# Optimization experiments

Hardware: AMD Instinct MI355X
Metric: run time of the kernel (lower is better)

Reference implementation:

```python
import jax, jax.numpy as jnp
import numpy as np

N, D, E_LOCAL, E_GLOBAL = 50000, 128, 500000, 600000


def gcn_conv(x, W, b, src, dst, w, n):
    """PyG GCNConv with add_self_loops=True, symmetric normalization.

    deg[i] = sum of incoming edge weights at i + 1 (self-loop weight 1)
    norm_e = deg^-1/2[src] * w_e * deg^-1/2[dst]
    out[i] = sum_e norm_e * (xW)[src_e]  +  deg^-1[i] * (xW)[i]  + b
    """
    xw = x @ W  # [n, out]
    deg = jax.ops.segment_sum(w, dst, num_segments=n) + 1.0
    dinv = jnp.where(deg > 0, jax.lax.rsqrt(deg), 0.0)
    norm = dinv[src] * w * dinv[dst]  # [E]
    agg = jax.ops.segment_sum(norm[:, None] * xw[src], dst, num_segments=n)
    self_loop = (dinv * dinv)[:, None] * xw
    return agg + self_loop + b


def setup_inputs() -> dict:
    key = jax.random.key(0)
    ks = jax.random.split(key, 10)
    activity = jax.random.normal(ks[0], (N, D), dtype=jnp.float32)
    learning = jax.random.normal(ks[1], (N, D), dtype=jnp.float32)
    edge_index = jax.random.randint(ks[2], (2, E_LOCAL), 0, N, dtype=jnp.int32)
    edge_weight = jax.random.uniform(ks[3], (E_LOCAL,), dtype=jnp.float32)
    global_edge_index = jax.random.randint(ks[4], (2, E_GLOBAL), 0, N, dtype=jnp.int32)
    global_edge_weight = jax.random.uniform(ks[5], (E_GLOBAL,), dtype=jnp.float32)
    s = 1.0 / np.sqrt(D)
    W_local = jax.random.uniform(ks[6], (D, D), jnp.float32, -s, s)
    b_local = jnp.zeros((D,), jnp.float32)
    W_global = jax.random.uniform(ks[7], (D, D), jnp.float32, -s, s)
    b_global = jnp.zeros((D,), jnp.float32)
    return {
        "activity": activity, "learning": learning,
        "edge_index": edge_index, "edge_weight": edge_weight,
        "global_edge_index": global_edge_index, "global_edge_weight": global_edge_weight,
        "W_local": W_local, "b_local": b_local,
        "W_global": W_global, "b_global": b_global,
    }


def reference(activity, learning, edge_index, edge_weight,
              global_edge_index, global_edge_weight,
              W_local, b_local, W_global, b_global):
    n = activity.shape[0]
    xa = activity + learning
    # Note: GCNConv1 branches in the original are dead code (outputs overwritten);
    # only GCNConv2 (local and global) affect the output.
    xl = gcn_conv(xa, W_local, b_local, edge_index[0], edge_index[1], edge_weight, n)
    xg = gcn_conv(xa, W_global, b_global, global_edge_index[0], global_edge_index[1], global_edge_weight, n)
    wei = jax.nn.sigmoid(xl + xg)
    return 2.0 * activity * wei + 2.0 * learning * (1.0 - wei)
```

## Files before the change

### kernel.cpp

```cpp
#include <hip/hip_runtime.h>

#define DFEAT 128
#define EPB 4096
#define MAXBINS 512

typedef __attribute__((ext_vector_type(8))) short short8;
typedef __attribute__((ext_vector_type(4))) float float4v;

__device__ __forceinline__ float bf2f(unsigned int h) {
    union { unsigned int u; float f; } v; v.u = h << 16; return v.f;
}
__device__ __forceinline__ unsigned short f2bf(float f) {
    union { float f; unsigned int u; } v; v.f = f;
    unsigned int u = v.u;
    unsigned int lsb = (u >> 16) & 1u;
    u += 0x7fffu + lsb;
    return (unsigned short)(u >> 16);
}
__device__ __forceinline__ float blo(unsigned int u) {
    union { unsigned int x; float f; } v; v.x = u << 16; return v.f;
}
__device__ __forceinline__ float bhi(unsigned int u) {
    union { unsigned int x; float f; } v; v.x = u & 0xffff0000u; return v.f;
}

__global__ __launch_bounds__(256) void zprep_kernel(
    const float* __restrict__ Wl, const float* __restrict__ Wg,
    unsigned short* __restrict__ WT,
    unsigned int* __restrict__ counts, int nz)
{
    if (blockIdx.x < 128) {
        int idx = blockIdx.x * 256 + threadIdx.x;
        int m = idx >> 14, rem = idx & 16383;
        int k = rem >> 7, c = rem & 127;
        const float* W = m ? Wg : Wl;
        WT[m * 16384 + c * 128 + k] = f2bf(W[k * 128 + c]);
        return;
    }
    int i = (blockIdx.x - 128) * 256 + threadIdx.x;
    if (i < nz) counts[i] = 0u;
}

__global__ __launch_bounds__(256) void gemm_bin1_kernel(
    const float* __restrict__ A, const float* __restrict__ L,
    const unsigned short* __restrict__ WT,
    unsigned short* __restrict__ xwl, unsigned short* __restrict__ xwg,
    const int* __restrict__ dstL, const int* __restrict__ dstG,
    unsigned int* __restrict__ counts,
    int El, int Eg, int n, int GB, int NPB)
{
    __shared__ unsigned int lcnt[MAXBINS];
    if (blockIdx.x >= GB) {
        const int NBINS = (2 * n + 255) >> 8;
        for (int b = threadIdx.x; b < NBINS; b += 256) lcnt[b] = 0u;
        __syncthreads();
        const int k = blockIdx.x - GB;
        const int e0 = k * EPB;
        const int E = El + Eg;
        #pragma unroll
        for (int r = 0; r < EPB / 256; ++r) {
            int e = e0 + r * 256 + threadIdx.x;
            if (e < E) {
                int t = (e < El) ? dstL[e] : n + dstG[e - El];
                atomicAdd(&lcnt[t >> 8], 1u);
            }
        }
        __syncthreads();
        for (int b = threadIdx.x; b < NBINS; b += 256)
            counts[(size_t)b * NPB + k] = lcnt[b];
        return;
    }
    const int tid  = threadIdx.x;
    const int wid  = tid >> 6;
    const int lane = tid & 63;
    const int quad = lane >> 4;
    const int cl   = lane & 15;

    int rowa = blockIdx.x * 64 + wid * 16 + cl;
    if (rowa > n - 1) rowa = n - 1;

    const float* Ar = A + (size_t)rowa * DFEAT;
    const float* Lr = L + (size_t)rowa * DFEAT;

    short8 a[4];
    #pragma unroll
    for (int kk = 0; kk < 4; ++kk) {
        const int kb = kk * 32 + quad * 8;
        float4 a0 = *(const float4*)&Ar[kb];
        float4 a1 = *(const float4*)&Ar[kb + 4];
        float4 l0 = *(const float4*)&Lr[kb];
        float4 l1 = *(const float4*)&Lr[kb + 4];
        union { short8 v; unsigned short u[8]; } s;
        s.u[0] = f2bf(a0.x + l0.x); s.u[1] = f2bf(a0.y + l0.y);
        s.u[2] = f2bf(a0.z + l0.z); s.u[3] = f2bf(a0.w + l0.w);
        s.u[4] = f2bf(a1.x + l1.x); s.u[5] = f2bf(a1.y + l1.y);
        s.u[6] = f2bf(a1.z + l1.z); s.u[7] = f2bf(a1.w + l1.w);
        a[kk] = s.v;
    }

    const int rbase = blockIdx.x * 64 + wid * 16 + quad * 4;
    const char* wtb = (const char*)WT + quad * 16;

    #pragma unroll
    for (int m = 0; m < 2; ++m) {
        unsigned short* out = m ? xwg : xwl;
        #pragma unroll
        for (int t = 0; t < 8; ++t) {
            const int col = t * 16 + cl;
            const char* bp = wtb + m * 32768 + col * 256;
            float4v acc = {0.f, 0.f, 0.f, 0.f};
            #pragma unroll
            for (int kk = 0; kk < 4; ++kk) {
                short8 b = *(const short8*)(bp + kk * 64);
                acc = __builtin_amdgcn_mfma_f32_16x16x32_bf16(a[kk], b, acc, 0, 0, 0);
            }
            #pragma unroll
            for (int r = 0; r < 4; ++r) {
                int ro = rbase + r;
                if (ro < n) out[(size_t)ro * DFEAT + col] = f2bf(acc[r]);
            }
        }
    }
}

__global__ __launch_bounds__(512) void scanA_kernel(unsigned int* __restrict__ counts,
                                                    unsigned int* __restrict__ bintot,
                                                    int NPB)
{
    __shared__ unsigned int tmp[512];
    const int b = blockIdx.x;
    const int i = threadIdx.x;
    unsigned int v = (i < NPB) ? counts[(size_t)b * NPB + i] : 0u;
    tmp[i] = v;
    __syncthreads();
    for (int off = 1; off < 512; off <<= 1) {
        unsigned int t = (i >= off) ? tmp[i - off] : 0u;
        __syncthreads();
        tmp[i] += t;
        __syncthreads();
    }
    if (i < NPB) counts[(size_t)b * NPB + i] = tmp[i] - v;
    if (i == 511) bintot[b] = tmp[511];
}

__global__ __launch_bounds__(512) void scanB_kernel(const unsigned int* __restrict__ bintot,
                                                    unsigned int* __restrict__ binbase,
                                                    int NBINS)
{
    __shared__ unsigned int tmp[512];
    const int i = threadIdx.x;
    unsigned int v = (i < NBINS) ? bintot[i] : 0u;
    tmp[i] = v;
    __syncthreads();
    for (int off = 1; off < 512; off <<= 1) {
        unsigned int t = (i >= off) ? tmp[i - off] : 0u;
        __syncthreads();
        tmp[i] += t;
        __syncthreads();
    }
    if (i < NBINS) binbase[i] = tmp[i] - v;
    if (i == 511) binbase[NBINS] = tmp[511];
}

__global__ __launch_bounds__(256) void scatter_kernel(
    const int* __restrict__ srcL, const int* __restrict__ dstL, const float* __restrict__ wL,
    const int* __restrict__ srcG, const int* __restrict__ dstG, const float* __restrict__ wG,
    const unsigned int* __restrict__ counts, const unsigned int* __restrict__ binbase,
    unsigned int* __restrict__ payload, unsigned char* __restrict__ tloc,
    int El, int Eg, int n, int NPB)
{
    __shared__ unsigned int lbase[MAXBINS];
    __shared__ unsigned int lcnt[MAXBINS];
    const int NBINS = (2 * n + 255) >> 8;
    const int k = blockIdx.x;
    for (int b = threadIdx.x; b < NBINS; b += 256) {
        lbase[b] = binbase[b] + counts[(size_t)b * NPB + k];
        lcnt[b]  = 0u;
    }
    __syncthreads();
    const int e0 = k * EPB;
    const int E = El + Eg;
    #pragma unroll
    for (int r = 0; r < EPB / 256; ++r) {
        int e = e0 + r * 256 + threadIdx.x;
        if (e < E) {
            int s, t; float w;
            if (e < El) { s = srcL[e]; t = dstL[e]; w = wL[e]; }
            else { int e2 = e - El; s = srcG[e2]; t = n + dstG[e2]; w = wG[e2]; }
            const int bin = t >> 8;
            unsigned int rank = atomicAdd(&lcnt[bin], 1u);
            unsigned int pos = lbase[bin] + rank;
            unsigned int wq = (unsigned int)(w * 65535.0f + 0.5f);
            if (wq > 65535u) wq = 65535u;
            payload[pos] = (wq << 16) | (unsigned int)s;
            tloc[pos] = (unsigned char)(t & 255);
        }
    }
}

__global__ __launch_bounds__(256) void binsort_kernel(
    const unsigned int* __restrict__ binbase,
    const unsigned int* __restrict__ payload, const unsigned char* __restrict__ tloc,
    unsigned int* __restrict__ edata, unsigned int* __restrict__ ptrpk,
    float* __restrict__ dinv, int n2)
{
    __shared__ unsigned int cnt[256], wsum[256], off[256], cnt2[256], tmp[256];
    const int b = blockIdx.x;
    const unsigned int s0 = binbase[b], s1 = binbase[b + 1];
    cnt[threadIdx.x] = 0u; wsum[threadIdx.x] = 0u; cnt2[threadIdx.x] = 0u;
    __syncthreads();
    for (unsigned int i = s0 + threadIdx.x; i < s1; i += 256) {
        unsigned int tl = tloc[i];
        atomicAdd(&cnt[tl], 1u);
        atomicAdd(&wsum[tl], payload[i] >> 16);
    }
    __syncthreads();
    unsigned int v = cnt[threadIdx.x];
    tmp[threadIdx.x] = v;
    __syncthreads();
    for (int o = 1; o < 256; o <<= 1) {
        unsigned int t = (threadIdx.x >= o) ? tmp[threadIdx.x - o] : 0u;
        __syncthreads();
        tmp[threadIdx.x] += t;
        __syncthreads();
    }
    off[threadIdx.x] = tmp[threadIdx.x] - v;
    const int t = b * 256 + threadIdx.x;
    if (t < n2) {
        dinv[t]  = rsqrtf((float)wsum[threadIdx.x] * (1.0f / 65535.0f) + 1.0f);
        ptrpk[t] = (s0 + off[threadIdx.x]) | (v << 24);
    }
    __syncthreads();
    for (unsigned int i = s0 + threadIdx.x; i < s1; i += 256) {
        unsigned int tl = tloc[i];
        unsigned int r = atomicAdd(&cnt2[tl], 1u);
        edata[s0 + off[tl] + r] = payload[i];
    }
}

__global__ __launch_bounds__(256) void gather_kernel(
    const unsigned short* __restrict__ xwl, const unsigned short* __restrict__ xwg,
    const unsigned int* __restrict__ ptrpk, const unsigned int* __restrict__ edata,
    const float* __restrict__ dinv,
    const float* __restrict__ A, const float* __restrict__ Lr,
    const float* __restrict__ bl, const float* __restrict__ bg,
    float* __restrict__ out, int n)
{
    const int lane = threadIdx.x & 63;
    const int grp  = lane >> 4;
    const int fl   = lane & 15;
    const int node = blockIdx.x * 4 + (threadIdx.x >> 6);
    if (node >= n) return;

    const unsigned int pl = ptrpk[node];
    const unsigned int pg = ptrpk[n + node];
    const int i0l = (int)(pl & 0xFFFFFFu);
    const int i1l = i0l + (int)(pl >> 24);
    const int i0g = (int)(pg & 0xFFFFFFu);
    const int i1g = i0g + (int)(pg >> 24);
    const float dvl = dinv[node];
    const float dvg = dinv[n + node];
    const float dl = dvl * dvl;
    const float dg = dvg * dvg;
    const float dtl = dvl * (1.0f / 65535.0f);
    const float dtg = dvg * (1.0f / 65535.0f);

    const int fo = fl * 8;
    const size_t nbase = (size_t)node * DFEAT + fo;
    const uint4 svl = *(const uint4*)&xwl[nbase];
    const uint4 svg = *(const uint4*)&xwg[nbase];

    float acc[8] = {0.f, 0.f, 0.f, 0.f, 0.f, 0.f, 0.f, 0.f};

    for (int b0 = i0l; b0 < i1l; b0 += 64) {
        int idx = b0 + lane;
        unsigned int ed = edata[idx < i1l ? idx : (i1l - 1)];
        int   sv  = (int)(ed & 0xFFFFu);
        float nmv = dinv[sv] * (float)(ed >> 16) * dtl;
        int cnt = i1l - b0; if (cnt > 64) cnt = 64;
        int iters = (cnt + 3) >> 2;
        #pragma unroll 4
        for (int jj = 0; jj < iters; ++jj) {
            int sl = 4 * jj + grp;
            float nm = __shfl(nmv, sl);
            int   s  = __shfl(sv,  sl);
            if (sl >= cnt) nm = 0.f;
            uint4 pk = *(const uint4*)&xwl[(size_t)s * DFEAT + fo];
            acc[0] += nm * blo(pk.x); acc[1] += nm * bhi(pk.x);
            acc[2] += nm * blo(pk.y); acc[3] += nm * bhi(pk.y);
            acc[4] += nm * blo(pk.z); acc[5] += nm * bhi(pk.z);
            acc[6] += nm * blo(pk.w); acc[7] += nm * bhi(pk.w);
        }
    }
    for (int b0 = i0g; b0 < i1g; b0 += 64) {
        int idx = b0 + lane;
        unsigned int ed = edata[idx < i1g ? idx : (i1g - 1)];
        int   sv  = (int)(ed & 0xFFFFu);
        float nmv = dinv[n + sv] * (float)(ed >> 16) * dtg;
        int cnt = i1g - b0; if (cnt > 64) cnt = 64;
        int iters = (cnt + 3) >> 2;
        #pragma unroll 4
        for (int jj = 0; jj < iters; ++jj) {
            int sl = 4 * jj + grp;
            float nm = __shfl(nmv, sl);
            int   s  = __shfl(sv,  sl);
            if (sl >= cnt) nm = 0.f;
            uint4 pk = *(const uint4*)&xwg[(size_t)s * DFEAT + fo];
            acc[0] += nm * blo(pk.x); acc[1] += nm * bhi(pk.x);
            acc[2] += nm * blo(pk.y); acc[3] += nm * bhi(pk.y);
            acc[4] += nm * blo(pk.z); acc[5] += nm * bhi(pk.z);
            acc[6] += nm * blo(pk.w); acc[7] += nm * bhi(pk.w);
        }
    }

    #pragma unroll
    for (int j = 0; j < 8; ++j) {
        acc[j] += __shfl_xor(acc[j], 16);
        acc[j] += __shfl_xor(acc[j], 32);
    }

    acc[0] += dl * blo(svl.x) + dg * blo(svg.x);
    acc[1] += dl * bhi(svl.x) + dg * bhi(svg.x);
    acc[2] += dl * blo(svl.y) + dg * blo(svg.y);
    acc[3] += dl * bhi(svl.y) + dg * bhi(svg.y);
    acc[4] += dl * blo(svl.z) + dg * blo(svg.z);
    acc[5] += dl * bhi(svl.z) + dg * bhi(svg.z);
    acc[6] += dl * blo(svl.w) + dg * blo(svg.w);
    acc[7] += dl * bhi(svl.w) + dg * bhi(svg.w);

    float s0a = (grp & 1) ? acc[2] : acc[0];
    float s1a = (grp & 1) ? acc[3] : acc[1];
    float s0b = (grp & 1) ? acc[6] : acc[4];
    float s1b = (grp & 1) ? acc[7] : acc[5];
    float v0 = (grp & 2) ? s0b : s0a;
    float v1 = (grp & 2) ? s1b : s1a;

    const int f0 = fo + grp * 2;
    const size_t obase = (size_t)node * DFEAT + f0;
    float2 b1 = *(const float2*)&bl[f0];
    float2 b2 = *(const float2*)&bg[f0];
    float2 a2 = *(const float2*)&A[obase];
    float2 l2 = *(const float2*)&Lr[obase];
    v0 += b1.x + b2.x;
    v1 += b1.y + b2.y;
    float w0 = 1.0f / (1.0f + __expf(-v0));
    float w1 = 1.0f / (1.0f + __expf(-v1));
    float o0 = 2.0f * (a2.x * w0 + l2.x * (1.0f - w0));
    float o1 = 2.0f * (a2.y * w1 + l2.y * (1.0f - w1));
    *(float2*)&out[obase] = make_float2(o0, o1);
}

extern "C" void kernel_launch(void* const* d_in, const int* in_sizes, int n_in,
                              void* d_out, int out_size, void* d_ws, size_t ws_size,
                              hipStream_t stream)
{
    const float* activity = (const float*)d_in[0];
    const float* learning = (const float*)d_in[1];
    const int*   ei  = (const int*)d_in[2];
    const float* ew  = (const float*)d_in[3];
    const int*   gei = (const int*)d_in[4];
    const float* gew = (const float*)d_in[5];
    const float* Wl  = (const float*)d_in[6];
    const float* bl  = (const float*)d_in[7];
    const float* Wg  = (const float*)d_in[8];
    const float* bg  = (const float*)d_in[9];

    const int n  = in_sizes[0] / DFEAT;
    const int El = in_sizes[3];
    const int Eg = in_sizes[5];
    const int n2 = 2 * n;
    const int E  = El + Eg;

    const int NPB   = (E + EPB - 1) / EPB;
    const int NBINS = (n2 + 255) / 256;

    char* ws = (char*)d_ws;
    const size_t xwB = (size_t)n * DFEAT * 2;
    size_t off = 0;
    unsigned short* xwl = (unsigned short*)(ws + off); off += xwB;
    unsigned short* xwg = (unsigned short*)(ws + off); off += xwB;
    float* dinv         = (float*)(ws + off);          off += (size_t)n2 * 4;
    unsigned int* ptrpk = (unsigned int*)(ws + off);   off += (size_t)n2 * 4;
    unsigned short* WT  = (unsigned short*)(ws + off); off += 65536;
    unsigned int* payload = (unsigned int*)(ws + off); off += (size_t)E * 4;
    unsigned char* tloc = (unsigned char*)(ws + off);  off += (size_t)((E + 3) & ~3);
    unsigned int* edata = (unsigned int*)(ws + off);   off += (size_t)E * 4;
    unsigned int* counts= (unsigned int*)(ws + off);   off += (size_t)NBINS * NPB * 4;
    unsigned int* bintot= (unsigned int*)(ws + off);   off += (size_t)NBINS * 4;
    unsigned int* binbase=(unsigned int*)(ws + off);   off += (size_t)(NBINS + 1) * 4;

    const int nz = NBINS * NPB;
    const int zb = (nz + 255) / 256;
    const int GB = (n + 63) / 64;

    zprep_kernel<<<dim3(128 + zb), dim3(256), 0, stream>>>(Wl, Wg, WT, counts, nz);

    gemm_bin1_kernel<<<dim3(GB + NPB), dim3(256), 0, stream>>>(
        activity, learning, WT, xwl, xwg,
        ei + El, gei + Eg, counts, El, Eg, n, GB, NPB);

    scanA_kernel<<<dim3(NBINS), dim3(512), 0, stream>>>(counts, bintot, NPB);
    scanB_kernel<<<dim3(1), dim3(512), 0, stream>>>(bintot, binbase, NBINS);

    scatter_kernel<<<dim3(NPB), dim3(256), 0, stream>>>(
        ei, ei + El, ew, gei, gei + Eg, gew,
        counts, binbase, payload, tloc, El, Eg, n, NPB);

    binsort_kernel<<<dim3(NBINS), dim3(256), 0, stream>>>(
        binbase, payload, tloc, edata, ptrpk, dinv, n2);

    gather_kernel<<<dim3((n + 3) / 4), dim3(256), 0, stream>>>(
        xwl, xwg, ptrpk, edata, dinv, activity, learning, bl, bg, (float*)d_out, n);
}
```

Baseline: 255.3 us.

## Fuse scan kernels, slim scatter payload, register-cached binsort, interleave local/global gather

Merges the two scan kernels into one, where the last block to finish (counted through an atomic counter) computes the bin bases. Scatter now reads only destinations and writes a single packed word of edge id plus local target, which drops the tloc byte array and the src/weight reads. Binsort looks up src and weight by edge id, keeps up to RMAX items per thread in registers to skip the second payload pass, and sums weights in float. The gather loop interleaves local and global edges in one loop for more memory-level parallelism. The cost is random gathers of src and weight inside binsort, plus an overflow fallback path.

New measurement: 291.3 us. +14.1%, slower.

```diff
diff --git a/kernel.cpp b/kernel.cpp
--- a/kernel.cpp
+++ b/kernel.cpp
@@ -3,6 +3,7 @@
 #define DFEAT 128
 #define EPB 4096
 #define MAXBINS 512
+#define RMAX 16
 
 typedef __attribute__((ext_vector_type(8))) short short8;
 typedef __attribute__((ext_vector_type(4))) float float4v;
@@ -123,11 +124,14 @@
     }
 }
 
-__global__ __launch_bounds__(512) void scanA_kernel(unsigned int* __restrict__ counts,
-                                                    unsigned int* __restrict__ bintot,
-                                                    int NPB)
+__global__ __launch_bounds__(512) void scanAB_kernel(unsigned int* __restrict__ counts,
+                                                     unsigned int* __restrict__ bintot,
+                                                     unsigned int* __restrict__ binbase,
+                                                     unsigned int* __restrict__ done,
+                                                     int NPB, int NBINS)
 {
     __shared__ unsigned int tmp[512];
+    __shared__ unsigned int tk;
     const int b = blockIdx.x;
     const int i = threadIdx.x;
     unsigned int v = (i < NPB) ? counts[(size_t)b * NPB + i] : 0u;
@@ -141,32 +145,30 @@
     }
     if (i < NPB) counts[(size_t)b * NPB + i] = tmp[i] - v;
     if (i == 511) bintot[b] = tmp[511];
-}
-
-__global__ __launch_bounds__(512) void scanB_kernel(const unsigned int* __restrict__ bintot,
-                                                    unsigned int* __restrict__ binbase,
-                                                    int NBINS)
-{
-    __shared__ unsigned int tmp[512];
-    const int i = threadIdx.x;
-    unsigned int v = (i < NBINS) ? bintot[i] : 0u;
-    tmp[i] = v;
-    __syncthreads();
-    for (int off = 1; off < 512; off <<= 1) {
-        unsigned int t = (i >= off) ? tmp[i - off] : 0u;
-        __syncthreads();
-        tmp[i] += t;
-        __syncthreads();
-    }
-    if (i < NBINS) binbase[i] = tmp[i] - v;
-    if (i == 511) binbase[NBINS] = tmp[511];
+    __threadfence();
+    __syncthreads();
+    if (i == 0) tk = atomicAdd(done, 1u);
+    __syncthreads();
+    if (tk == (unsigned int)(NBINS - 1)) {
+        __threadfence();
+        unsigned int v2 = (i < NBINS) ? bintot[i] : 0u;
+        tmp[i] = v2;
+        __syncthreads();
+        for (int off = 1; off < 512; off <<= 1) {
+            unsigned int t = (i >= off) ? tmp[i - off] : 0u;
+            __syncthreads();
+            tmp[i] += t;
+            __syncthreads();
+        }
+        if (i < NBINS) binbase[i] = tmp[i] - v2;
+        if (i == NBINS - 1) binbase[NBINS] = tmp[i];
+    }
 }
 
 __global__ __launch_bounds__(256) void scatter_kernel(
-    const int* __restrict__ srcL, const int* __restrict__ dstL, const float* __restrict__ wL,
-    const int* __restrict__ srcG, const int* __restrict__ dstG, const float* __restrict__ wG,
+    const int* __restrict__ dstL, const int* __restrict__ dstG,
     const unsigned int* __restrict__ counts, const unsigned int* __restrict__ binbase,
-    unsigned int* __restrict__ payload, unsigned char* __restrict__ tloc,
+    unsigned int* __restrict__ payload,
     int El, int Eg, int n, int NPB)
 {
     __shared__ unsigned int lbase[MAXBINS];
@@ -184,57 +186,99 @@
     for (int r = 0; r < EPB / 256; ++r) {
         int e = e0 + r * 256 + threadIdx.x;
         if (e < E) {
-            int s, t; float w;
-            if (e < El) { s = srcL[e]; t = dstL[e]; w = wL[e]; }
-            else { int e2 = e - El; s = srcG[e2]; t = n + dstG[e2]; w = wG[e2]; }
+            int t = (e < El) ? dstL[e] : n + dstG[e - El];
             const int bin = t >> 8;
             unsigned int rank = atomicAdd(&lcnt[bin], 1u);
-            unsigned int pos = lbase[bin] + rank;
+            payload[lbase[bin] + rank] = ((unsigned int)e << 8) | (unsigned int)(t & 255);
+        }
+    }
+}
+
+__global__ __launch_bounds__(256) void binsort_kernel(
+    const unsigned int* __restrict__ binbase, const unsigned int* __restrict__ payload,
+    const int* __restrict__ srcL, const float* __restrict__ wL,
+    const int* __restrict__ srcG, const float* __restrict__ wG,
+    unsigned int* __restrict__ edata, unsigned int* __restrict__ ptrpk,
+    float* __restrict__ dinv, int El, int n2)
+{
+    __shared__ unsigned int cnt[256], off[256], cnt2[256], tmp[256];
+    __shared__ float wsumf[256];
+    __shared__ int sovf;
+    const int b = blockIdx.x;
+    const unsigned int s0 = binbase[b], s1 = binbase[b + 1];
+    const int tid = threadIdx.x;
+    cnt[tid] = 0u; cnt2[tid] = 0u; wsumf[tid] = 0.f;
+    if (tid == 0) sovf = 0;
+    __syncthreads();
+
+    unsigned int payA[RMAX];
+    unsigned int rank[RMAX];
+    float        wv[RMAX];
+
+    #pragma unroll
+    for (int it = 0; it < RMAX; ++it) {
+        unsigned int i = s0 + (unsigned int)(it * 256 + tid);
+        if (i < s1) {
+            unsigned int p = payload[i];
+            payA[it] = p;
+            unsigned int e = p >> 8, tl = p & 255u;
+            float w = (e < (unsigned int)El) ? wL[e] : wG[e - El];
+            wv[it] = w;
+            rank[it] = atomicAdd(&cnt[tl], 1u);
+            atomicAdd(&wsumf[tl], w);
+        }
+    }
+    for (unsigned int i = s0 + (unsigned int)(RMAX * 256 + tid); i < s1; i += 256) {
+        sovf = 1;
+        unsigned int p = payload[i];
+        unsigned int e = p >> 8, tl = p & 255u;
+        float w = (e < (unsigned int)El) ? wL[e] : wG[e - El];
+        atomicAdd(&cnt[tl], 1u);
+        atomicAdd(&wsumf[tl], w);
+    }
+    __syncthreads();
+
+    unsigned int v = cnt[tid];
+    tmp[tid] = v;
+    __syncthreads();
+    for (int o = 1; o < 256; o <<= 1) {
+        unsigned int t = (tid >= o) ? tmp[tid - o] : 0u;
+        __syncthreads();
+        tmp[tid] += t;
+        __syncthreads();
+    }
+    off[tid] = tmp[tid] - v;
+    const int t = b * 256 + tid;
+    if (t < n2) {
+        dinv[t]  = rsqrtf(wsumf[tid] + 1.0f);
+        ptrpk[t] = (s0 + off[tid]) | (v << 24);
+    }
+    __syncthreads();
+
+    if (!sovf) {
+        #pragma unroll
+        for (int it = 0; it < RMAX; ++it) {
+            unsigned int i = s0 + (unsigned int)(it * 256 + tid);
+            if (i < s1) {
+                unsigned int p = payA[it];
+                unsigned int e = p >> 8, tl = p & 255u;
+                int src = (e < (unsigned int)El) ? srcL[e] : srcG[e - El];
+                unsigned int wq = (unsigned int)(wv[it] * 65535.0f + 0.5f);
+                if (wq > 65535u) wq = 65535u;
+                edata[s0 + off[tl] + rank[it]] = (wq << 16) | (unsigned int)src;
+            }
+        }
+    } else {
+        for (unsigned int i = s0 + tid; i < s1; i += 256) {
+            unsigned int p = payload[i];
+            unsigned int e = p >> 8, tl = p & 255u;
+            int src = (e < (unsigned int)El) ? srcL[e] : srcG[e - El];
+            float w = (e < (unsigned int)El) ? wL[e] : wG[e - El];
             unsigned int wq = (unsigned int)(w * 65535.0f + 0.5f);
             if (wq > 65535u) wq = 65535u;
-            payload[pos] = (wq << 16) | (unsigned int)s;
-            tloc[pos] = (unsigned char)(t & 255);
-        }
-    }
-}
-
-__global__ __launch_bounds__(256) void binsort_kernel(
-    const unsigned int* __restrict__ binbase,
-    const unsigned int* __restrict__ payload, const unsigned char* __restrict__ tloc,
-    unsigned int* __restrict__ edata, unsigned int* __restrict__ ptrpk,
-    float* __restrict__ dinv, int n2)
-{
-    __shared__ unsigned int cnt[256], wsum[256], off[256], cnt2[256], tmp[256];
-    const int b = blockIdx.x;
-    const unsigned int s0 = binbase[b], s1 = binbase[b + 1];
-    cnt[threadIdx.x] = 0u; wsum[threadIdx.x] = 0u; cnt2[threadIdx.x] = 0u;
-    __syncthreads();
-    for (unsigned int i = s0 + threadIdx.x; i < s1; i += 256) {
-        unsigned int tl = tloc[i];
-        atomicAdd(&cnt[tl], 1u);
-        atomicAdd(&wsum[tl], payload[i] >> 16);
-    }
-    __syncthreads();
-    unsigned int v = cnt[threadIdx.x];
-    tmp[threadIdx.x] = v;
-    __syncthreads();
-    for (int o = 1; o < 256; o <<= 1) {
-        unsigned int t = (threadIdx.x >= o) ? tmp[threadIdx.x - o] : 0u;
-        __syncthreads();
-        tmp[threadIdx.x] += t;
-        __syncthreads();
-    }
-    off[threadIdx.x] = tmp[threadIdx.x] - v;
-    const int t = b * 256 + threadIdx.x;
-    if (t < n2) {
-        dinv[t]  = rsqrtf((float)wsum[threadIdx.x] * (1.0f / 65535.0f) + 1.0f);
-        ptrpk[t] = (s0 + off[threadIdx.x]) | (v << 24);
-    }
-    __syncthreads();
-    for (unsigned int i = s0 + threadIdx.x; i < s1; i += 256) {
-        unsigned int tl = tloc[i];
-        unsigned int r = atomicAdd(&cnt2[tl], 1u);
-        edata[s0 + off[tl] + r] = payload[i];
+            unsigned int r = atomicAdd(&cnt2[tl], 1u);
+            edata[s0 + off[tl] + r] = (wq << 16) | (unsigned int)src;
+        }
     }
 }
 
@@ -254,10 +298,8 @@
 
     const unsigned int pl = ptrpk[node];
     const unsigned int pg = ptrpk[n + node];
-    const int i0l = (int)(pl & 0xFFFFFFu);
-    const int i1l = i0l + (int)(pl >> 24);
-    const int i0g = (int)(pg & 0xFFFFFFu);
-    const int i1g = i0g + (int)(pg >> 24);
+    int bl_ = (int)(pl & 0xFFFFFFu);  int nl_ = (int)(pl >> 24);
+    int bg_ = (int)(pg & 0xFFFFFFu);  int ng_ = (int)(pg >> 24);
     const float dvl = dinv[node];
     const float dvg = dinv[n + node];
     const float dl = dvl * dvl;
@@ -272,45 +314,50 @@
 
     float acc[8] = {0.f, 0.f, 0.f, 0.f, 0.f, 0.f, 0.f, 0.f};
 
-    for (int b0 = i0l; b0 < i1l; b0 += 64) {
-        int idx = b0 + lane;
-        unsigned int ed = edata[idx < i1l ? idx : (i1l - 1)];
-        int   sv  = (int)(ed & 0xFFFFu);
-        float nmv = dinv[sv] * (float)(ed >> 16) * dtl;
-        int cnt = i1l - b0; if (cnt > 64) cnt = 64;
-        int iters = (cnt + 3) >> 2;
-        #pragma unroll 4
-        for (int jj = 0; jj < iters; ++jj) {
-            int sl = 4 * jj + grp;
-            float nm = __shfl(nmv, sl);
-            int   s  = __shfl(sv,  sl);
-            if (sl >= cnt) nm = 0.f;
-            uint4 pk = *(const uint4*)&xwl[(size_t)s * DFEAT + fo];
-            acc[0] += nm * blo(pk.x); acc[1] += nm * bhi(pk.x);
-            acc[2] += nm * blo(pk.y); acc[3] += nm * bhi(pk.y);
-            acc[4] += nm * blo(pk.z); acc[5] += nm * bhi(pk.z);
-            acc[6] += nm * blo(pk.w); acc[7] += nm * bhi(pk.w);
-        }
-    }
-    for (int b0 = i0g; b0 < i1g; b0 += 64) {
-        int idx = b0 + lane;
-        unsigned int ed = edata[idx < i1g ? idx : (i1g - 1)];
-        int   sv  = (int)(ed & 0xFFFFu);
-        float nmv = dinv[n + sv] * (float)(ed >> 16) * dtg;
-        int cnt = i1g - b0; if (cnt > 64) cnt = 64;
-        int iters = (cnt + 3) >> 2;
-        #pragma unroll 4
-        for (int jj = 0; jj < iters; ++jj) {
-            int sl = 4 * jj + grp;
-            float nm = __shfl(nmv, sl);
-            int   s  = __shfl(sv,  sl);
-            if (sl >= cnt) nm = 0.f;
-            uint4 pk = *(const uint4*)&xwg[(size_t)s * DFEAT + fo];
-            acc[0] += nm * blo(pk.x); acc[1] += nm * bhi(pk.x);
-            acc[2] += nm * blo(pk.y); acc[3] += nm * bhi(pk.y);
-            acc[4] += nm * blo(pk.z); acc[5] += nm * bhi(pk.z);
-            acc[6] += nm * blo(pk.w); acc[7] += nm * bhi(pk.w);
-        }
+    while (nl_ > 0 || ng_ > 0) {
+        const int cl_ = nl_ > 64 ? 64 : nl_;
+        const int cg_ = ng_ > 64 ? 64 : ng_;
+        float nml = 0.f; int sL = 0;
+        if (cl_ > 0) {
+            unsigned int ed = edata[bl_ + (lane < cl_ ? lane : cl_ - 1)];
+            sL  = (int)(ed & 0xFFFFu);
+            nml = dinv[sL] * (float)(ed >> 16) * dtl;
+        }
+        float nmg = 0.f; int sG = 0;
+        if (cg_ > 0) {
+            unsigned int ed = edata[bg_ + (lane < cg_ ? lane : cg_ - 1)];
+            sG  = (int)(ed & 0xFFFFu);
+            nmg = dinv[n + sG] * (float)(ed >> 16) * dtg;
+        }
+        const int itl = (cl_ + 3) >> 2;
+        const int itg = (cg_ + 3) >> 2;
+        const int itm = itl > itg ? itl : itg;
+        #pragma unroll 2
+        for (int jj = 0; jj < itm; ++jj) {
+            const int sl = 4 * jj + grp;
+            if (4 * jj < cl_) {
+                float nm = __shfl(nml, sl);
+                int   s  = __shfl(sL, sl);
+                if (sl >= cl_) nm = 0.f;
+                uint4 pk = *(const uint4*)&xwl[(size_t)s * DFEAT + fo];
+                acc[0] += nm * blo(pk.x); acc[1] += nm * bhi(pk.x);
+                acc[2] += nm * blo(pk.y); acc[3] += nm * bhi(pk.y);
+                acc[4] += nm * blo(pk.z); acc[5] += nm * bhi(pk.z);
+                acc[6] += nm * blo(pk.w); acc[7] += nm * bhi(pk.w);
+            }
+            if (4 * jj < cg_) {
+                float nm = __shfl(nmg, sl);
+                int   s  = __shfl(sG, sl);
+                if (sl >= cg_) nm = 0.f;
+                uint4 pk = *(const uint4*)&xwg[(size_t)s * DFEAT + fo];
+                acc[0] += nm * blo(pk.x); acc[1] += nm * bhi(pk.x);
+                acc[2] += nm * blo(pk.y); acc[3] += nm * bhi(pk.y);
+                acc[4] += nm * blo(pk.z); acc[5] += nm * bhi(pk.z);
+                acc[6] += nm * blo(pk.w); acc[7] += nm * bhi(pk.w);
+            }
+        }
+        bl_ += cl_;  nl_ -= cl_;
+        bg_ += cg_;  ng_ -= cg_;
     }
 
     #pragma unroll
@@ -383,13 +430,13 @@
     unsigned int* ptrpk = (unsigned int*)(ws + off);   off += (size_t)n2 * 4;
     unsigned short* WT  = (unsigned short*)(ws + off); off += 65536;
     unsigned int* payload = (unsigned int*)(ws + off); off += (size_t)E * 4;
-    unsigned char* tloc = (unsigned char*)(ws + off);  off += (size_t)((E + 3) & ~3);
     unsigned int* edata = (unsigned int*)(ws + off);   off += (size_t)E * 4;
-    unsigned int* counts= (unsigned int*)(ws + off);   off += (size_t)NBINS * NPB * 4;
+    unsigned int* counts= (unsigned int*)(ws + off);   off += ((size_t)NBINS * NPB + 1) * 4;
+    unsigned int* done  = counts + (size_t)NBINS * NPB;
     unsigned int* bintot= (unsigned int*)(ws + off);   off += (size_t)NBINS * 4;
     unsigned int* binbase=(unsigned int*)(ws + off);   off += (size_t)(NBINS + 1) * 4;
 
-    const int nz = NBINS * NPB;
+    const int nz = NBINS * NPB + 1;
     const int zb = (nz + 255) / 256;
     const int GB = (n + 63) / 64;
 
@@ -399,15 +446,13 @@
         activity, learning, WT, xwl, xwg,
         ei + El, gei + Eg, counts, El, Eg, n, GB, NPB);
 
-    scanA_kernel<<<dim3(NBINS), dim3(512), 0, stream>>>(counts, bintot, NPB);
-    scanB_kernel<<<dim3(1), dim3(512), 0, stream>>>(bintot, binbase, NBINS);
+    scanAB_kernel<<<dim3(NBINS), dim3(512), 0, stream>>>(counts, bintot, binbase, done, NPB, NBINS);
 
     scatter_kernel<<<dim3(NPB), dim3(256), 0, stream>>>(
-        ei, ei + El, ew, gei, gei + Eg, gew,
-        counts, binbase, payload, tloc, El, Eg, n, NPB);
+        ei + El, gei + Eg, counts, binbase, payload, El, Eg, n, NPB);
 
     binsort_kernel<<<dim3(NBINS), dim3(256), 0, stream>>>(
-        binbase, payload, tloc, edata, ptrpk, dinv, n2);
+        binbase, payload, ei, ew, gei, gew, edata, ptrpk, dinv, El, n2);
 
     gather_kernel<<<dim3((n + 3) / 4), dim3(256), 0, stream>>>(
         xwl, xwg, ptrpk, edata, dinv, activity, learning, bl, bg, (float*)d_out, n);
```

## Fuse two-level scan kernels, drop counts zeroing, keep binsort payload in registers

Applied to the files above, without the earlier changes.

Merges the per-bin scan and the bin-total scan into one kernel: the last block to finish, found with a global atomic ticket, scans the bin totals. This removes one kernel launch. The zeroing of the counts array is dropped, which relies on the binning kernel writing every entry, so only the done counter is reset. Binsort now keeps up to 16 payload entries per thread in registers, together with their local ranks, so the final scatter does not re-read payload and tloc or run a second round of atomics. If a bin overflows that capacity it falls back to the old path. The cost is higher register pressure and a threadfence-based last-block pattern.

Measured after the change: 297.9 us. 16.7% more time.

```diff
diff --git a/kernel.cpp b/kernel.cpp
--- a/kernel.cpp
+++ b/kernel.cpp
@@ -3,6 +3,7 @@
 #define DFEAT 128
 #define EPB 4096
 #define MAXBINS 512
+#define RMAX 16
 
 typedef __attribute__((ext_vector_type(8))) short short8;
 typedef __attribute__((ext_vector_type(4))) float float4v;
@@ -27,7 +28,7 @@
 __global__ __launch_bounds__(256) void zprep_kernel(
     const float* __restrict__ Wl, const float* __restrict__ Wg,
     unsigned short* __restrict__ WT,
-    unsigned int* __restrict__ counts, int nz)
+    unsigned int* __restrict__ done)
 {
     if (blockIdx.x < 128) {
         int idx = blockIdx.x * 256 + threadIdx.x;
@@ -37,8 +38,7 @@
         WT[m * 16384 + c * 128 + k] = f2bf(W[k * 128 + c]);
         return;
     }
-    int i = (blockIdx.x - 128) * 256 + threadIdx.x;
-    if (i < nz) counts[i] = 0u;
+    if (threadIdx.x == 0) *done = 0u;
 }
 
 __global__ __launch_bounds__(256) void gemm_bin1_kernel(
@@ -123,11 +123,14 @@
     }
 }
 
-__global__ __launch_bounds__(512) void scanA_kernel(unsigned int* __restrict__ counts,
-                                                    unsigned int* __restrict__ bintot,
-                                                    int NPB)
+__global__ __launch_bounds__(512) void scanAB_kernel(unsigned int* __restrict__ counts,
+                                                     unsigned int* __restrict__ bintot,
+                                                     unsigned int* __restrict__ binbase,
+                                                     unsigned int* __restrict__ done,
+                                                     int NPB, int NBINS)
 {
     __shared__ unsigned int tmp[512];
+    __shared__ unsigned int tk;
     const int b = blockIdx.x;
     const int i = threadIdx.x;
     unsigned int v = (i < NPB) ? counts[(size_t)b * NPB + i] : 0u;
@@ -141,25 +144,24 @@
     }
     if (i < NPB) counts[(size_t)b * NPB + i] = tmp[i] - v;
     if (i == 511) bintot[b] = tmp[511];
-}
-
-__global__ __launch_bounds__(512) void scanB_kernel(const unsigned int* __restrict__ bintot,
-                                                    unsigned int* __restrict__ binbase,
-                                                    int NBINS)
-{
-    __shared__ unsigned int tmp[512];
-    const int i = threadIdx.x;
-    unsigned int v = (i < NBINS) ? bintot[i] : 0u;
-    tmp[i] = v;
-    __syncthreads();
-    for (int off = 1; off < 512; off <<= 1) {
-        unsigned int t = (i >= off) ? tmp[i - off] : 0u;
-        __syncthreads();
-        tmp[i] += t;
-        __syncthreads();
-    }
-    if (i < NBINS) binbase[i] = tmp[i] - v;
-    if (i == 511) binbase[NBINS] = tmp[511];
+    __threadfence();
+    __syncthreads();
+    if (i == 0) tk = atomicAdd(done, 1u);
+    __syncthreads();
+    if (tk == (unsigned int)(NBINS - 1)) {
+        __threadfence();
+        unsigned int v2 = (i < NBINS) ? bintot[i] : 0u;
+        tmp[i] = v2;
+        __syncthreads();
+        for (int off = 1; off < 512; off <<= 1) {
+            unsigned int t = (i >= off) ? tmp[i - off] : 0u;
+            __syncthreads();
+            tmp[i] += t;
+            __syncthreads();
+        }
+        if (i < NBINS) binbase[i] = tmp[i] - v2;
+        if (i == NBINS - 1) binbase[NBINS] = tmp[i];
+    }
 }
 
 __global__ __launch_bounds__(256) void scatter_kernel(
@@ -204,37 +206,72 @@
     unsigned int* __restrict__ edata, unsigned int* __restrict__ ptrpk,
     float* __restrict__ dinv, int n2)
 {
-    __shared__ unsigned int cnt[256], wsum[256], off[256], cnt2[256], tmp[256];
+    __shared__ unsigned int cnt[256], off2[256], tmp[256], wsum[256];
+    __shared__ int sovf;
     const int b = blockIdx.x;
     const unsigned int s0 = binbase[b], s1 = binbase[b + 1];
-    cnt[threadIdx.x] = 0u; wsum[threadIdx.x] = 0u; cnt2[threadIdx.x] = 0u;
-    __syncthreads();
-    for (unsigned int i = s0 + threadIdx.x; i < s1; i += 256) {
+    const int tid = threadIdx.x;
+    cnt[tid] = 0u; wsum[tid] = 0u;
+    if (tid == 0) sovf = 0;
+    __syncthreads();
+
+    unsigned int payA[RMAX];
+    unsigned int rt[RMAX];
+
+    #pragma unroll
+    for (int it = 0; it < RMAX; ++it) {
+        unsigned int i = s0 + (unsigned int)(it * 256 + tid);
+        if (i < s1) {
+            unsigned int p = payload[i];
+            unsigned int tl = tloc[i];
+            payA[it] = p;
+            unsigned int r = atomicAdd(&cnt[tl], 1u);
+            atomicAdd(&wsum[tl], p >> 16);
+            rt[it] = r | (tl << 16);
+        }
+    }
+    for (unsigned int i = s0 + (unsigned int)(RMAX * 256 + tid); i < s1; i += 256) {
+        sovf = 1;
+        unsigned int p = payload[i];
         unsigned int tl = tloc[i];
         atomicAdd(&cnt[tl], 1u);
-        atomicAdd(&wsum[tl], payload[i] >> 16);
-    }
-    __syncthreads();
-    unsigned int v = cnt[threadIdx.x];
-    tmp[threadIdx.x] = v;
+        atomicAdd(&wsum[tl], p >> 16);
+    }
+    __syncthreads();
+
+    unsigned int v = cnt[tid];
+    tmp[tid] = v;
     __syncthreads();
     for (int o = 1; o < 256; o <<= 1) {
-        unsigned int t = (threadIdx.x >= o) ? tmp[threadIdx.x - o] : 0u;
-        __syncthreads();
-        tmp[threadIdx.x] += t;
-        __syncthreads();
-    }
-    off[threadIdx.x] = tmp[threadIdx.x] - v;
-    const int t = b * 256 + threadIdx.x;
+        unsigned int t = (tid >= o) ? tmp[tid - o] : 0u;
+        __syncthreads();
+        tmp[tid] += t;
+        __syncthreads();
+    }
+    off2[tid] = tmp[tid] - v;
+    const int t = b * 256 + tid;
     if (t < n2) {
-        dinv[t]  = rsqrtf((float)wsum[threadIdx.x] * (1.0f / 65535.0f) + 1.0f);
-        ptrpk[t] = (s0 + off[threadIdx.x]) | (v << 24);
-    }
-    __syncthreads();
-    for (unsigned int i = s0 + threadIdx.x; i < s1; i += 256) {
-        unsigned int tl = tloc[i];
-        unsigned int r = atomicAdd(&cnt2[tl], 1u);
-        edata[s0 + off[tl] + r] = payload[i];
+        dinv[t]  = rsqrtf((float)wsum[tid] * (1.0f / 65535.0f) + 1.0f);
+        ptrpk[t] = (s0 + off2[tid]) | (v << 24);
+    }
+    __syncthreads();
+
+    if (!sovf) {
+        #pragma unroll
+        for (int it = 0; it < RMAX; ++it) {
+            unsigned int i = s0 + (unsigned int)(it * 256 + tid);
+            if (i < s1)
+                edata[s0 + off2[rt[it] >> 16] + (rt[it] & 0xFFFFu)] = payA[it];
+        }
+    } else {
+        tmp[tid] = 0u;
+        __syncthreads();
+        for (unsigned int i = s0 + tid; i < s1; i += 256) {
+            unsigned int p = payload[i];
+            unsigned int tl = tloc[i];
+            unsigned int r = atomicAdd(&tmp[tl], 1u);
+            edata[s0 + off2[tl] + r] = p;
+        }
     }
 }
 
@@ -385,22 +422,20 @@
     unsigned int* payload = (unsigned int*)(ws + off); off += (size_t)E * 4;
     unsigned char* tloc = (unsigned char*)(ws + off);  off += (size_t)((E + 3) & ~3);
     unsigned int* edata = (unsigned int*)(ws + off);   off += (size_t)E * 4;
-    unsigned int* counts= (unsigned int*)(ws + off);   off += (size_t)NBINS * NPB * 4;
+    unsigned int* counts= (unsigned int*)(ws + off);   off += ((size_t)NBINS * NPB + 1) * 4;
+    unsigned int* done  = counts + (size_t)NBINS * NPB;
     unsigned int* bintot= (unsigned int*)(ws + off);   off += (size_t)NBINS * 4;
     unsigned int* binbase=(unsigned int*)(ws + off);   off += (size_t)(NBINS + 1) * 4;
 
-    const int nz = NBINS * NPB;
-    const int zb = (nz + 255) / 256;
     const int GB = (n + 63) / 64;
 
-    zprep_kernel<<<dim3(128 + zb), dim3(256), 0, stream>>>(Wl, Wg, WT, counts, nz);
+    zprep_kernel<<<dim3(129), dim3(256), 0, stream>>>(Wl, Wg, WT, done);
 
     gemm_bin1_kernel<<<dim3(GB + NPB), dim3(256), 0, stream>>>(
         activity, learning, WT, xwl, xwg,
         ei + El, gei + Eg, counts, El, Eg, n, GB, NPB);
 
-    scanA_kernel<<<dim3(NBINS), dim3(512), 0, stream>>>(counts, bintot, NPB);
-    scanB_kernel<<<dim3(1), dim3(512), 0, stream>>>(bintot, binbase, NBINS);
+    scanAB_kernel<<<dim3(NBINS), dim3(512), 0, stream>>>(counts, bintot, binbase, done, NPB, NBINS);
 
     scatter_kernel<<<dim3(NPB), dim3(256), 0, stream>>>(
         ei, ei + El, ew, gei, gei + Eg, gew,
```
